# Performance work log

Hardware: AMD Instinct MI355X
Metric: run time of the kernel (lower is better)

Reference implementation:

```python
import math
import jax, jax.numpy as jnp
import numpy as np

B, T, C, HS = 4, 4096, 2048, 128

def setup_inputs() -> dict:
    key = jax.random.key(0)
    k1, k2, k3, k4 = jax.random.split(key, 4)
    x = jax.random.normal(k1, (B, T, C), dtype=jnp.float32)
    # torch Linear init ~ U(-1/sqrt(in), 1/sqrt(in)); normal*0.02 is fine for a numeric baseline
    Wq = jax.random.normal(k2, (C, HS), dtype=jnp.float32) * 0.02
    Wk = jax.random.normal(k3, (C, HS), dtype=jnp.float32) * 0.02
    Wv = jax.random.normal(k4, (C, HS), dtype=jnp.float32) * 0.02
    return {"x": x, "Wq": Wq, "Wk": Wk, "Wv": Wv}

def reference(x, Wq, Wk, Wv):
    # Single-head causal self-attention (dropout in eval mode = identity).
    q = x @ Wq          # [B,T,HS]
    k = x @ Wk          # [B,T,HS]
    v = x @ Wv          # [B,T,HS]
    scale = 1.0 / math.sqrt(HS)
    att = jnp.einsum('bqd,bkd->bqk', q, k) * scale          # [B,T,T]
    causal = jnp.tril(jnp.ones((T, T), dtype=bool))          # [T,T]
    att = jnp.where(causal[None, :, :], att, -jnp.inf)
    att = jax.nn.softmax(att, axis=-1)
    y = jnp.einsum('bqk,bkd->bqd', att, v)                   # [B,T,HS]
    return y
```

## Files before the change

kernel.cpp:

```cpp
#include <hip/hip_runtime.h>
#include <hip/hip_bf16.h>


#define B_  4
#define T_  4096
#define C_  2048
#define HS_ 128

typedef unsigned short u16;
typedef __attribute__((ext_vector_type(8))) short short8;
typedef __attribute__((ext_vector_type(4))) float floatx4;

static __device__ __forceinline__ u16 f2bf(float x) {
  union { float f; unsigned u; } c; c.f = x;
  unsigned r = 0x7fffu + ((c.u >> 16) & 1u);
  return (u16)((c.u + r) >> 16);
}

__global__ __launch_bounds__(256) void wtrans3_kernel(
    const float* __restrict__ Wq, const float* __restrict__ Wk,
    const float* __restrict__ Wv, u16* __restrict__ dst) {
  __shared__ u16 tile[32][33];
  int z = blockIdx.z;
  const float* src = (z == 0) ? Wq : (z == 1) ? Wk : Wv;
  u16* d = dst + (size_t)z * HS_ * C_;
  int c0 = blockIdx.x * 32, r0 = blockIdx.y * 32;
  int tx = threadIdx.x, ty = threadIdx.y;
#pragma unroll
  for (int i = 0; i < 4; ++i)
    tile[ty + 8 * i][tx] = f2bf(src[(size_t)(r0 + ty + 8 * i) * HS_ + (c0 + tx)]);
  __syncthreads();
#pragma unroll
  for (int i = 0; i < 4; ++i)
    d[(size_t)(c0 + ty + 8 * i) * C_ + (r0 + tx)] = tile[tx][ty + 8 * i];
}

#define GBM 128
#define GBK 64
#define NKT (C_ / GBK)
#define XP 72
#define TP 136

__global__ __launch_bounds__(256, 2) void qkv_gemm_kernel(
    const float* __restrict__ X, const u16* __restrict__ WT3,
    u16* __restrict__ qkv, u16* __restrict__ vT) {
  __shared__ u16 smem[2 * 2 * GBM * XP];
  u16 (*Xs)[GBM][XP] = (u16(*)[GBM][XP])smem;
  u16 (*Ws)[GBM][XP] = (u16(*)[GBM][XP])(smem + 2 * GBM * XP);

  int z = blockIdx.y;
  const u16* Wt = WT3 + (size_t)z * HS_ * C_;
  int t = threadIdx.x;
  int wv = t >> 6, lane = t & 63;
  int l15 = lane & 15, hi = lane >> 4;
  int wm = (wv & 1) * 64;
  int wn = (wv >> 1) * 64;
  size_t mbase = (size_t)blockIdx.x * GBM;

  int srow = t >> 3, sc = t & 7;
  const float* xrowp[4];
  const u16* wrowp[4];
#pragma unroll
  for (int i = 0; i < 4; ++i) {
    xrowp[i] = &X[(mbase + i * 32 + srow) * C_];
    wrowp[i] = &Wt[(size_t)(i * 32 + srow) * C_];
  }

  floatx4 acc[4][4];
#pragma unroll
  for (int i = 0; i < 4; ++i)
#pragma unroll
    for (int j = 0; j < 4; ++j) acc[i][j] = (floatx4){0.f, 0.f, 0.f, 0.f};

  floatx4 xreg[4][2];
  short8 wreg[4];

  {
    int koff = sc * 8;
#pragma unroll
    for (int i = 0; i < 4; ++i) {
      xreg[i][0] = *(const floatx4*)&xrowp[i][koff];
      xreg[i][1] = *(const floatx4*)&xrowp[i][koff + 4];
      wreg[i] = *(const short8*)&wrowp[i][koff];
    }
  }
#pragma unroll
  for (int i = 0; i < 4; ++i) {
    short8 xv;
#pragma unroll
    for (int j = 0; j < 4; ++j) {
      xv[j] = (short)f2bf(xreg[i][0][j]);
      xv[4 + j] = (short)f2bf(xreg[i][1][j]);
    }
    *(short8*)&Xs[0][i * 32 + srow][sc * 8] = xv;
    *(short8*)&Ws[0][i * 32 + srow][sc * 8] = wreg[i];
  }
  __syncthreads();

  for (int kt = 0; kt < NKT; ++kt) {
    int p = kt & 1;
    if (kt + 1 < NKT) {
      int koff = (kt + 1) * GBK + sc * 8;
#pragma unroll
      for (int i = 0; i < 4; ++i) {
        xreg[i][0] = *(const floatx4*)&xrowp[i][koff];
        xreg[i][1] = *(const floatx4*)&xrowp[i][koff + 4];
        wreg[i] = *(const short8*)&wrowp[i][koff];
      }
    }

#pragma unroll
    for (int ks = 0; ks < 2; ++ks) {
      short8 af[4], bf[4];
#pragma unroll
      for (int mt = 0; mt < 4; ++mt)
        af[mt] = *(const short8*)&Xs[p][wm + mt * 16 + l15][ks * 32 + hi * 8];
#pragma unroll
      for (int nt = 0; nt < 4; ++nt)
        bf[nt] = *(const short8*)&Ws[p][wn + nt * 16 + l15][ks * 32 + hi * 8];
#pragma unroll
      for (int mt = 0; mt < 4; ++mt)
#pragma unroll
        for (int nt = 0; nt < 4; ++nt)
          acc[mt][nt] = __builtin_amdgcn_mfma_f32_16x16x32_bf16(
              af[mt], bf[nt], acc[mt][nt], 0, 0, 0);
    }

    if (kt + 1 < NKT) {
#pragma unroll
      for (int i = 0; i < 4; ++i) {
        short8 xv;
#pragma unroll
        for (int j = 0; j < 4; ++j) {
          xv[j] = (short)f2bf(xreg[i][0][j]);
          xv[4 + j] = (short)f2bf(xreg[i][1][j]);
        }
        *(short8*)&Xs[p ^ 1][i * 32 + srow][sc * 8] = xv;
        *(short8*)&Ws[p ^ 1][i * 32 + srow][sc * 8] = wreg[i];
      }
    }
    __syncthreads();
  }

  if (z != 2) {
    u16* outp = qkv + (size_t)z * ((size_t)B_ * T_ * HS_);
#pragma unroll
    for (int mt = 0; mt < 4; ++mt)
#pragma unroll
      for (int nt = 0; nt < 4; ++nt)
#pragma unroll
        for (int r = 0; r < 4; ++r) {
          size_t row = mbase + wm + mt * 16 + hi * 4 + r;
          int col = wn + nt * 16 + l15;
          outp[row * HS_ + col] = f2bf(acc[mt][nt][r]);
        }
  } else {
    u16 (*Tb)[TP] = (u16(*)[TP])smem;
#pragma unroll
    for (int mt = 0; mt < 4; ++mt)
#pragma unroll
      for (int nt = 0; nt < 4; ++nt)
#pragma unroll
        for (int r = 0; r < 4; ++r)
          Tb[wn + nt * 16 + l15][wm + mt * 16 + hi * 4 + r] = f2bf(acc[mt][nt][r]);
    __syncthreads();
    int b = (int)(mbase >> 12);
    int trow0 = (int)(mbase & (T_ - 1));
    u16* vb = vT + (size_t)b * HS_ * T_;
#pragma unroll
    for (int i = 0; i < 8; ++i) {
      int id = i * 256 + t;
      int c = id >> 4, ch = id & 15;
      short8 v = *(const short8*)&Tb[c][ch * 8];
      *(short8*)&vb[(size_t)c * T_ + trow0 + ch * 8] = v;
    }
  }
}

#define BQ 64
#define BKV 64
#define CHUNK 16

template <bool WRITE_PARTIAL>
static __device__ __forceinline__ void flash_body(
    const u16* __restrict__ q, const u16* __restrict__ k,
    const u16* __restrict__ vT, float* __restrict__ outO,
    float* __restrict__ Mp, float* __restrict__ Lp,
    int b, int qb, int kb0, int kb1, int slot) {
  __shared__ u16 Ks[BKV][136];
  __shared__ u16 Vs[144][72];
  __shared__ u16 Ps[BQ][72];
  int t = threadIdx.x;
  int wv = t >> 6, lane = t & 63, l15 = lane & 15, hi = lane >> 4;

  const float sc = 0.08838834764831845f * 1.4426950408889634f;

  short8 qf[4];
  {
    const u16* qrow = q + (size_t)(b * T_ + qb * BQ + wv * 16 + l15) * HS_;
#pragma unroll
    for (int ks = 0; ks < 4; ++ks)
      qf[ks] = *(const short8*)(qrow + ks * 32 + hi * 8);
  }

  {
    int r = 128 + (t >> 4), c0 = (t & 15) * 4;
    const u16 one = 0x3F80;
    Vs[r][c0] = one; Vs[r][c0 + 1] = one;
    Vs[r][c0 + 2] = one; Vs[r][c0 + 3] = one;
  }

  floatx4 of[9];
#pragma unroll
  for (int dt = 0; dt < 9; ++dt) of[dt] = (floatx4){0.f, 0.f, 0.f, 0.f};
  float m_run[4];
#pragma unroll
  for (int r = 0; r < 4; ++r) m_run[r] = -__builtin_inff();

  const u16* kbase = k + (size_t)b * T_ * HS_;
  const u16* vbase = vT + (size_t)b * HS_ * T_;

  short8 kreg[4], vreg[4];
#pragma unroll
  for (int i = 0; i < 4; ++i) {
    int id = i * 256 + t;
    int n = id >> 4, ck = id & 15;
    kreg[i] = *(const short8*)&kbase[(size_t)(kb0 * BKV + n) * HS_ + ck * 8];
    int d = id >> 3, cv = id & 7;
    vreg[i] = *(const short8*)&vbase[(size_t)d * T_ + kb0 * BKV + cv * 8];
  }

  for (int kb = kb0; kb <= kb1; ++kb) {
#pragma unroll
    for (int i = 0; i < 4; ++i) {
      int id = i * 256 + t;
      int n = id >> 4, ck = id & 15;
      *(short8*)&Ks[n][ck * 8] = kreg[i];
      int d = id >> 3, cv = id & 7;
      *(short8*)&Vs[d][cv * 8] = vreg[i];
    }
    __syncthreads();

    if (kb < kb1) {
#pragma unroll
      for (int i = 0; i < 4; ++i) {
        int id = i * 256 + t;
        int n = id >> 4, ck = id & 15;
        kreg[i] = *(const short8*)&kbase[(size_t)((kb + 1) * BKV + n) * HS_ + ck * 8];
        int d = id >> 3, cv = id & 7;
        vreg[i] = *(const short8*)&vbase[(size_t)d * T_ + (kb + 1) * BKV + cv * 8];
      }
    }

    floatx4 sf[4];
#pragma unroll
    for (int nt = 0; nt < 4; ++nt) {
      floatx4 s = (floatx4){0.f, 0.f, 0.f, 0.f};
#pragma unroll
      for (int ks = 0; ks < 4; ++ks) {
        short8 bfrag = *(const short8*)&Ks[nt * 16 + l15][ks * 32 + hi * 8];
        s = __builtin_amdgcn_mfma_f32_16x16x32_bf16(qf[ks], bfrag, s, 0, 0, 0);
      }
      sf[nt] = s;
    }

    float sv[4][4];
    if (kb == qb) {
#pragma unroll
      for (int nt = 0; nt < 4; ++nt) {
        int col = nt * 16 + l15;
#pragma unroll
        for (int r = 0; r < 4; ++r) {
          int row = wv * 16 + hi * 4 + r;
          sv[nt][r] = (col <= row) ? sf[nt][r] * sc : -__builtin_inff();
        }
      }
    } else {
#pragma unroll
      for (int nt = 0; nt < 4; ++nt)
#pragma unroll
        for (int r = 0; r < 4; ++r) sv[nt][r] = sf[nt][r] * sc;
    }

    float mt4[4];
#pragma unroll
    for (int r = 0; r < 4; ++r)
      mt4[r] = fmaxf(fmaxf(sv[0][r], sv[1][r]), fmaxf(sv[2][r], sv[3][r]));
#pragma unroll
    for (int off = 1; off < 16; off <<= 1)
#pragma unroll
      for (int r = 0; r < 4; ++r)
        mt4[r] = fmaxf(mt4[r], __shfl_xor(mt4[r], off));

    bool need = false;
#pragma unroll
    for (int r = 0; r < 4; ++r) need = need || (mt4[r] > m_run[r] + 8.f);
    if (__any(need)) {
      float alpha[4];
#pragma unroll
      for (int r = 0; r < 4; ++r) {
        float mn = fmaxf(m_run[r], mt4[r]);
        alpha[r] = exp2f(m_run[r] - mn);
        m_run[r] = mn;
      }
#pragma unroll
      for (int dt = 0; dt < 9; ++dt)
#pragma unroll
        for (int r = 0; r < 4; ++r) of[dt][r] *= alpha[r];
    }

    float pv[4][4];
#pragma unroll
    for (int nt = 0; nt < 4; ++nt)
#pragma unroll
      for (int r = 0; r < 4; ++r) pv[nt][r] = exp2f(sv[nt][r] - m_run[r]);

#pragma unroll
    for (int nt = 0; nt < 4; ++nt)
#pragma unroll
      for (int r = 0; r < 4; ++r)
        Ps[wv * 16 + hi * 4 + r][nt * 16 + l15] = f2bf(pv[nt][r]);
    __asm__ volatile("s_waitcnt lgkmcnt(0)" ::: "memory");

#pragma unroll
    for (int ks2 = 0; ks2 < 2; ++ks2) {
      short8 af = *(const short8*)&Ps[wv * 16 + l15][ks2 * 32 + hi * 8];
#pragma unroll
      for (int dt = 0; dt < 9; ++dt) {
        short8 bfrag = *(const short8*)&Vs[dt * 16 + l15][ks2 * 32 + hi * 8];
        of[dt] = __builtin_amdgcn_mfma_f32_16x16x32_bf16(af, bfrag, of[dt], 0, 0, 0);
      }
    }
    __syncthreads();
  }

  if (WRITE_PARTIAL) {
    float* Op = outO + (size_t)slot * (BQ * HS_);
#pragma unroll
    for (int dt = 0; dt < 8; ++dt)
#pragma unroll
      for (int r = 0; r < 4; ++r) {
        int row = wv * 16 + hi * 4 + r;
        Op[row * HS_ + dt * 16 + l15] = of[dt][r];
      }
    if (l15 == 0) {
#pragma unroll
      for (int r = 0; r < 4; ++r) {
        int row = wv * 16 + hi * 4 + r;
        Mp[slot * BQ + row] = m_run[r];
        Lp[slot * BQ + row] = of[8][r];
      }
    }
  } else {
    float rl[4];
#pragma unroll
    for (int r = 0; r < 4; ++r) rl[r] = 1.0f / of[8][r];
#pragma unroll
    for (int dt = 0; dt < 8; ++dt)
#pragma unroll
      for (int r = 0; r < 4; ++r) {
        size_t row = (size_t)(b * T_ + qb * BQ + wv * 16 + hi * 4 + r);
        outO[row * HS_ + dt * 16 + l15] = of[dt][r] * rl[r];
      }
  }
}

__global__ __launch_bounds__(256, 3) void flash_partial_kernel(
    const u16* __restrict__ q, const u16* __restrict__ k,
    const u16* __restrict__ vT, float* __restrict__ Opart,
    float* __restrict__ Mpart, float* __restrict__ Lpart) {
  int qb = blockIdx.x, c = blockIdx.y, b = blockIdx.z;
  int kb0 = c * CHUNK;
  if (kb0 > qb) return;
  int kb1 = min(qb, kb0 + CHUNK - 1);
  int slot = (b * (T_ / BQ) + qb) * 4 + c;
  flash_body<true>(q, k, vT, Opart, Mpart, Lpart, b, qb, kb0, kb1, slot);
}

__global__ __launch_bounds__(256, 3) void flash_attn_kernel(
    const u16* __restrict__ q, const u16* __restrict__ k,
    const u16* __restrict__ vT, float* __restrict__ out) {
  int qb = blockIdx.x, b = blockIdx.y;
  flash_body<false>(q, k, vT, out, nullptr, nullptr, b, qb, 0, qb, 0);
}

__global__ __launch_bounds__(256) void flash_merge_kernel(
    const float* __restrict__ Opart, const float* __restrict__ Mpart,
    const float* __restrict__ Lpart, float* __restrict__ out) {
  __shared__ float w[4][BQ];
  __shared__ float invL[BQ];
  int qb = blockIdx.x, b = blockIdx.y;
  int t = threadIdx.x;
  int nch = qb / CHUNK + 1;
  int slot0 = (b * (T_ / BQ) + qb) * 4;

  if (t < BQ) {
    float mv[4], mmax = -__builtin_inff();
    for (int c = 0; c < nch; ++c) {
      mv[c] = Mpart[(slot0 + c) * BQ + t];
      mmax = fmaxf(mmax, mv[c]);
    }
    float L = 0.f;
    for (int c = 0; c < nch; ++c) {
      float wc = exp2f(mv[c] - mmax);
      w[c][t] = wc;
      L += wc * Lpart[(slot0 + c) * BQ + t];
    }
    invL[t] = 1.0f / L;
  }
  __syncthreads();

  size_t obase = ((size_t)(b * T_) + (size_t)qb * BQ) * HS_;
#pragma unroll
  for (int j = 0; j < 32; ++j) {
    int e = j * 256 + t;
    int row = e >> 7;
    float acc = 0.f;
    for (int c = 0; c < nch; ++c)
      acc += w[c][row] * Opart[(size_t)(slot0 + c) * (BQ * HS_) + e];
    out[obase + e] = acc * invL[row];
  }
}

extern "C" void kernel_launch(void* const* d_in, const int* in_sizes, int n_in,
                              void* d_out, int out_size, void* d_ws, size_t ws_size,
                              hipStream_t stream) {
  const float* x  = (const float*)d_in[0];
  const float* Wq = (const float*)d_in[1];
  const float* Wk = (const float*)d_in[2];
  const float* Wv = (const float*)d_in[3];
  float* out = (float*)d_out;

  u16* ws = (u16*)d_ws;
  const size_t wtsz  = (size_t)HS_ * C_;
  const size_t qkvsz = (size_t)B_ * T_ * HS_;
  u16* WT = ws;
  u16* qv = WT + 3 * wtsz;
  u16* kv = qv + qkvsz;
  u16* vT = kv + qkvsz;
  const size_t base_bytes = (3 * wtsz + 3 * qkvsz) * sizeof(u16);

  const int NSLOT = B_ * (T_ / BQ) * 4;
  float* Opart = (float*)((char*)d_ws + base_bytes);
  float* Mpart = Opart + (size_t)NSLOT * BQ * HS_;
  float* Lpart = Mpart + (size_t)NSLOT * BQ;
  const size_t split_bytes =
      base_bytes + ((size_t)NSLOT * BQ * HS_ + 2 * (size_t)NSLOT * BQ) * sizeof(float);

  dim3 tb(32, 8);
  wtrans3_kernel<<<dim3(HS_ / 32, C_ / 32, 3), tb, 0, stream>>>(Wq, Wk, Wv, WT);

  qkv_gemm_kernel<<<dim3((B_ * T_) / GBM, 3), 256, 0, stream>>>(x, WT, qv, vT);

  if (ws_size >= split_bytes) {
    flash_partial_kernel<<<dim3(T_ / BQ, 4, B_), 256, 0, stream>>>(
        qv, kv, vT, Opart, Mpart, Lpart);
    flash_merge_kernel<<<dim3(T_ / BQ, B_), 256, 0, stream>>>(
        Opart, Mpart, Lpart, out);
  } else {
    flash_attn_kernel<<<dim3(T_ / BQ, B_), 256, 0, stream>>>(qv, kv, vT, out);
  }
}
```

Before: 322.2 us.

## Deepen QKV projection GEMM prefetch to two register stages ahead

The projection GEMM main loop now keeps two sets of prefetch registers and issues global loads two K-tiles ahead, unrolling the loop by two over the LDS double buffer. Sched barriers pin the global loads ahead of the MFMA phase. The aim is to hide global memory latency better in the x@W projection. In exchange it roughly doubles prefetch register usage, which may lower occupancy, and it assumes NKT is even.

```diff
diff --git a/kernel.cpp b/kernel.cpp
--- a/kernel.cpp
+++ b/kernel.cpp
@@ -72,75 +72,73 @@
 #pragma unroll
     for (int j = 0; j < 4; ++j) acc[i][j] = (floatx4){0.f, 0.f, 0.f, 0.f};
 
-  floatx4 xreg[4][2];
-  short8 wreg[4];
-
-  {
-    int koff = sc * 8;
-#pragma unroll
-    for (int i = 0; i < 4; ++i) {
-      xreg[i][0] = *(const floatx4*)&xrowp[i][koff];
-      xreg[i][1] = *(const floatx4*)&xrowp[i][koff + 4];
-      wreg[i] = *(const short8*)&wrowp[i][koff];
-    }
-  }
-#pragma unroll
-  for (int i = 0; i < 4; ++i) {
-    short8 xv;
-#pragma unroll
-    for (int j = 0; j < 4; ++j) {
-      xv[j] = (short)f2bf(xreg[i][0][j]);
-      xv[4 + j] = (short)f2bf(xreg[i][1][j]);
-    }
-    *(short8*)&Xs[0][i * 32 + srow][sc * 8] = xv;
-    *(short8*)&Ws[0][i * 32 + srow][sc * 8] = wreg[i];
-  }
+  floatx4 xA[4][2]; short8 wA[4];
+  floatx4 xB[4][2]; short8 wB[4];
+
+#define ISSUE(Xr, Wr, KT)                                        \
+  do {                                                           \
+    int koff = (KT) * GBK + sc * 8;                              \
+    _Pragma("unroll") for (int i = 0; i < 4; ++i) {              \
+      Xr[i][0] = *(const floatx4*)&xrowp[i][koff];               \
+      Xr[i][1] = *(const floatx4*)&xrowp[i][koff + 4];           \
+      Wr[i] = *(const short8*)&wrowp[i][koff];                   \
+    }                                                            \
+  } while (0)
+
+#define STAGE(P, Xr, Wr)                                         \
+  do {                                                           \
+    _Pragma("unroll") for (int i = 0; i < 4; ++i) {              \
+      short8 xv;                                                 \
+      _Pragma("unroll") for (int j = 0; j < 4; ++j) {            \
+        xv[j] = (short)f2bf(Xr[i][0][j]);                        \
+        xv[4 + j] = (short)f2bf(Xr[i][1][j]);                    \
+      }                                                          \
+      *(short8*)&Xs[P][i * 32 + srow][sc * 8] = xv;              \
+      *(short8*)&Ws[P][i * 32 + srow][sc * 8] = Wr[i];           \
+    }                                                            \
+  } while (0)
+
+#define MFMA_PHASE(P)                                                         \
+  do {                                                                        \
+    _Pragma("unroll") for (int ks = 0; ks < 2; ++ks) {                        \
+      short8 af[4], bf[4];                                                    \
+      _Pragma("unroll") for (int mt = 0; mt < 4; ++mt)                        \
+        af[mt] = *(const short8*)&Xs[P][wm + mt * 16 + l15][ks * 32 + hi * 8];\
+      _Pragma("unroll") for (int nt = 0; nt < 4; ++nt)                        \
+        bf[nt] = *(const short8*)&Ws[P][wn + nt * 16 + l15][ks * 32 + hi * 8];\
+      _Pragma("unroll") for (int mt = 0; mt < 4; ++mt)                        \
+        _Pragma("unroll") for (int nt = 0; nt < 4; ++nt)                      \
+          acc[mt][nt] = __builtin_amdgcn_mfma_f32_16x16x32_bf16(              \
+              af[mt], bf[nt], acc[mt][nt], 0, 0, 0);                          \
+    }                                                                         \
+  } while (0)
+
+  ISSUE(xA, wA, 0);
+  ISSUE(xB, wB, 1);
+  STAGE(0, xA, wA);
   __syncthreads();
 
-  for (int kt = 0; kt < NKT; ++kt) {
-    int p = kt & 1;
-    if (kt + 1 < NKT) {
-      int koff = (kt + 1) * GBK + sc * 8;
-#pragma unroll
-      for (int i = 0; i < 4; ++i) {
-        xreg[i][0] = *(const floatx4*)&xrowp[i][koff];
-        xreg[i][1] = *(const floatx4*)&xrowp[i][koff + 4];
-        wreg[i] = *(const short8*)&wrowp[i][koff];
-      }
-    }
-
-#pragma unroll
-    for (int ks = 0; ks < 2; ++ks) {
-      short8 af[4], bf[4];
-#pragma unroll
-      for (int mt = 0; mt < 4; ++mt)
-        af[mt] = *(const short8*)&Xs[p][wm + mt * 16 + l15][ks * 32 + hi * 8];
-#pragma unroll
-      for (int nt = 0; nt < 4; ++nt)
-        bf[nt] = *(const short8*)&Ws[p][wn + nt * 16 + l15][ks * 32 + hi * 8];
-#pragma unroll
-      for (int mt = 0; mt < 4; ++mt)
-#pragma unroll
-        for (int nt = 0; nt < 4; ++nt)
-          acc[mt][nt] = __builtin_amdgcn_mfma_f32_16x16x32_bf16(
-              af[mt], bf[nt], acc[mt][nt], 0, 0, 0);
-    }
-
-    if (kt + 1 < NKT) {
-#pragma unroll
-      for (int i = 0; i < 4; ++i) {
-        short8 xv;
-#pragma unroll
-        for (int j = 0; j < 4; ++j) {
-          xv[j] = (short)f2bf(xreg[i][0][j]);
-          xv[4 + j] = (short)f2bf(xreg[i][1][j]);
-        }
-        *(short8*)&Xs[p ^ 1][i * 32 + srow][sc * 8] = xv;
-        *(short8*)&Ws[p ^ 1][i * 32 + srow][sc * 8] = wreg[i];
-      }
-    }
+  for (int kt = 0; kt < NKT; kt += 2) {
+    if (kt + 2 < NKT) {
+      ISSUE(xA, wA, kt + 2);
+      __builtin_amdgcn_sched_barrier(0);
+    }
+    MFMA_PHASE(0);
+    STAGE(1, xB, wB);
     __syncthreads();
-  }
+
+    if (kt + 3 < NKT) {
+      ISSUE(xB, wB, kt + 3);
+      __builtin_amdgcn_sched_barrier(0);
+    }
+    MFMA_PHASE(1);
+    if (kt + 2 < NKT) STAGE(0, xA, wA);
+    __syncthreads();
+  }
+
+#undef ISSUE
+#undef STAGE
+#undef MFMA_PHASE
 
   if (z != 2) {
     u16* outp = qkv + (size_t)z * ((size_t)B_ * T_ * HS_);
```

New measurement: 323.0 us. Within noise of the previous version (+0.2%).
